# Optimization experiments

Measured on AMD Instinct MI355X. Metric: run time of the kernel, lower is better.

## Reference

```python
import jax, jax.numpy as jnp
import numpy as np
import math

FACTOR = 5


def setup_inputs() -> dict:
    key = jax.random.key(0)
    k1, k2, k3, k4 = jax.random.split(key, 4)
    B, L, H, D = 8, 1024, 8, 64
    S = FACTOR * math.ceil(math.log(L))  # U_part = 35
    return {
        "queries": jax.random.normal(k1, (B, L, H, D), jnp.float32),
        "keys": jax.random.normal(k2, (B, L, H, D), jnp.float32),
        "values": jax.random.normal(k3, (B, L, H, D), jnp.float32),
        "sample_idx": jax.random.randint(k4, (L, S), 0, L, dtype=jnp.int32),
        "attn_mask": 0,  # unused by the original forward
    }


def reference(queries, keys, values, sample_idx, attn_mask):
    B, L_Q, H, D = queries.shape
    L_K = keys.shape[1]
    # [B, L, H, D] -> [B, H, L, D]
    Q = jnp.transpose(queries, (0, 2, 1, 3))
    K = jnp.transpose(keys, (0, 2, 1, 3))
    V = jnpp_transpose(values) if False else jnp.transpose(values, (0, 2, 1, 3))

    u = min(FACTOR * math.ceil(math.log(L_Q)), L_Q)  # n_top

    # --- _prob_QK: sampled scores, sparsity measure, top-u query selection ---
    K_sample = K[:, :, sample_idx, :]  # [B, H, L_Q, S, D]
    QK_sample = jnp.einsum('bhqd,bhqsd->bhqs', Q, K_sample)  # [B, H, L_Q, S]
    M = QK_sample.max(axis=-1) - QK_sample.sum(axis=-1) / L_K  # [B, H, L_Q]
    _, M_top = jax.lax.top_k(M, u)  # [B, H, u]

    Q_reduce = jnp.take_along_axis(Q, M_top[..., None], axis=2)  # [B, H, u, D]
    scale = 1.0 / math.sqrt(D)
    scores_top = jnp.einsum('bhud,bhkd->bhuk', Q_reduce, K) * scale  # [B, H, u, L_K]

    # --- initial context (mask_flag=True): running causal mean of V ---
    denom = jnp.arange(1, L_K + 1, dtype=V.dtype)[:, None]  # [L_K, 1]
    context = jnp.cumsum(V, axis=2) / denom  # [B, H, L_K, D]

    # --- softmax over keys, sparse update of selected query rows ---
    attn = jax.nn.softmax(scores_top, axis=-1)  # [B, H, u, L_K]
    update = jnp.einsum('bhuk,bhkd->bhud', attn, V)  # [B, H, u, D]

    b_idx = jnp.arange(B)[:, None, None]
    h_idx = jnp.arange(H)[None, :, None]
    context = context.at[b_idx, h_idx, M_top].set(update)

    return jnp.transpose(context, (0, 2, 1, 3))  # [B, L_Q, H, D]
```

## Files before the change

### kernel.cpp

```cpp
#include <hip/hip_runtime.h>
#include <math.h>

#define BB 8
#define LL 1024
#define HH 8
#define DD 64
#define SS 35
#define UU 35
#define BH (BB*HH)
#define NCHK 4
#define CHK 256
#define RPAD 48

#define CSBLOCKS BH
#define MBLOCKS (BB*LL)

typedef __attribute__((ext_vector_type(8))) short short8;
typedef __attribute__((ext_vector_type(4))) float f32x4;

__device__ __forceinline__ size_t qkv_off(int b, int l, int h, int d) {
    return (((size_t)b*LL + l)*HH + h)*DD + d;
}

__device__ __forceinline__ unsigned short f2bf(float x) {
    unsigned int u = __float_as_uint(x);
    u = (u + 0x7fffu + ((u >> 16) & 1u)) >> 16;
    return (unsigned short)u;
}

__device__ __forceinline__ short8 ld_bf8_g(const float* __restrict__ p) {
    float4 x = *reinterpret_cast<const float4*>(p);
    float4 y = *reinterpret_cast<const float4*>(p + 4);
    short8 r;
    r[0] = (short)f2bf(x.x); r[1] = (short)f2bf(x.y);
    r[2] = (short)f2bf(x.z); r[3] = (short)f2bf(x.w);
    r[4] = (short)f2bf(y.x); r[5] = (short)f2bf(y.y);
    r[6] = (short)f2bf(y.z); r[7] = (short)f2bf(y.w);
    return r;
}

__device__ __forceinline__ float red8_shr(float p) {
    int t;
    t = __builtin_amdgcn_update_dpp(0, __float_as_int(p), 0x111, 0xF, 0xF, true);
    p += __int_as_float(t);
    t = __builtin_amdgcn_update_dpp(0, __float_as_int(p), 0x112, 0xF, 0xF, true);
    p += __int_as_float(t);
    t = __builtin_amdgcn_update_dpp(0, __float_as_int(p), 0x114, 0xF, 0xF, true);
    p += __int_as_float(t);
    return p;
}

__device__ __forceinline__ float wave_fmax64(float x) {
    int t;
    t = __builtin_amdgcn_update_dpp(0, __float_as_int(x), 0xB1, 0xF, 0xF, true);
    x = fmaxf(x, __int_as_float(t));
    t = __builtin_amdgcn_update_dpp(0, __float_as_int(x), 0x4E, 0xF, 0xF, true);
    x = fmaxf(x, __int_as_float(t));
    t = __builtin_amdgcn_update_dpp(0, __float_as_int(x), 0x141, 0xF, 0xF, true);
    x = fmaxf(x, __int_as_float(t));
    t = __builtin_amdgcn_update_dpp(0, __float_as_int(x), 0x140, 0xF, 0xF, true);
    x = fmaxf(x, __int_as_float(t));
    x = fmaxf(x, __shfl_xor(x, 16));
    x = fmaxf(x, __shfl_xor(x, 32));
    return x;
}

__device__ __forceinline__ int wave_imin64(int x) {
    int t;
    t = __builtin_amdgcn_update_dpp(0, x, 0xB1, 0xF, 0xF, true);  x = (t < x) ? t : x;
    t = __builtin_amdgcn_update_dpp(0, x, 0x4E, 0xF, 0xF, true);  x = (t < x) ? t : x;
    t = __builtin_amdgcn_update_dpp(0, x, 0x141, 0xF, 0xF, true); x = (t < x) ? t : x;
    t = __builtin_amdgcn_update_dpp(0, x, 0x140, 0xF, 0xF, true); x = (t < x) ? t : x;
    int y;
    y = __shfl_xor(x, 16); x = (y < x) ? y : x;
    y = __shfl_xor(x, 32); x = (y < x) ? y : x;
    return x;
}

__global__ __launch_bounds__(512, 2) void kernel_M_cumsum(const float* __restrict__ Q,
                                                          const float* __restrict__ K,
                                                          const float* __restrict__ V,
                                                          const int*   __restrict__ sidx,
                                                          float* __restrict__ M,
                                                          float* __restrict__ out) {
    int blk = blockIdx.x;
    if (blk < CSBLOCKS) {
        __shared__ float partial[8][64];
        int bh = blk;
        int b = bh >> 3, h = bh & 7;
        int d = threadIdx.x & 63, seg = threadIdx.x >> 6;
        int l0 = seg * 128;
        const float* vp = V + qkv_off(b, l0, h, d);

        float s = 0.f;
#pragma unroll 8
        for (int i = 0; i < 128; i++) s += vp[(size_t)i * (HH * DD)];
        partial[seg][d] = s;
        __syncthreads();
        float run = 0.f;
#pragma unroll
        for (int ss = 0; ss < 7; ss++) {
            float v = partial[ss][d];
            run += (ss < seg) ? v : 0.f;
        }
        float* op = out + qkv_off(b, l0, h, d);
#pragma unroll 8
        for (int i = 0; i < 128; i++) {
            run += vp[(size_t)i * (HH * DD)];
            op[(size_t)i * (HH * DD)] = run / (float)(l0 + i + 1);
        }
    } else {
        __shared__ float s_mx[8][8];
        __shared__ float s_sm[8][8];
        int mblk = blk - CSBLOCKS;
        int b = mblk & 7;
        int q = mblk >> 3;
        int tid = threadIdx.x;
        int w = tid >> 6, lane = tid & 63;
        int h = lane >> 3, j = lane & 7, dsub = j * 4;

        const float* qb = Q + ((size_t)(b * LL + q) * HH + h) * DD + dsub;
        f32x4 q0 = *reinterpret_cast<const f32x4*>(qb);
        f32x4 q1 = *reinterpret_cast<const f32x4*>(qb + 32);

        const int* sq = sidx + q * SS;
        int sl[5];
#pragma unroll
        for (int i = 0; i < 5; i++) {
            int s = w + 8 * i;
            sl[i] = sq[s < SS ? s : 0];
        }

        const float* kbase = K + (size_t)b * (LL * HH * DD) + h * DD + dsub;
        f32x4 ka[5], kc[5];
#pragma unroll
        for (int i = 0; i < 5; i++) {
            const float* kp = kbase + (size_t)sl[i] * (HH * DD);
            ka[i] = *reinterpret_cast<const f32x4*>(kp);
            kc[i] = *reinterpret_cast<const f32x4*>(kp + 32);
        }

        float mx = -INFINITY, sm = 0.f;
#pragma unroll
        for (int i = 0; i < 5; i++) {
            float d = q0.x * ka[i].x + q0.y * ka[i].y + q0.z * ka[i].z + q0.w * ka[i].w
                    + q1.x * kc[i].x + q1.y * kc[i].y + q1.z * kc[i].z + q1.w * kc[i].w;
            d = red8_shr(d);
            bool valid = (i < 4) || (w < 3);
            if (valid) { mx = fmaxf(mx, d); sm += d; }
        }
        if (j == 7) { s_mx[w][h] = mx; s_sm[w][h] = sm; }
        __syncthreads();
        if (tid < 8) {
            float m2 = -INFINITY, s2 = 0.f;
#pragma unroll
            for (int ww = 0; ww < 8; ww++) {
                m2 = fmaxf(m2, s_mx[ww][tid]);
                s2 += s_sm[ww][tid];
            }
            M[(b * HH + tid) * LL + q] = m2 - s2 * (1.0f / LL);
        }
    }
}

__global__ __launch_bounds__(256) void kernel_attn_part(const float* __restrict__ Q,
                                                        const float* __restrict__ K,
                                                        const float* __restrict__ V,
                                                        const float* __restrict__ M,
                                                        int*   __restrict__ top,
                                                        float* __restrict__ m_ws,
                                                        float* __restrict__ se_ws,
                                                        float* __restrict__ pv_ws) {
    __shared__ unsigned short vt[64 * CHK];
    __shared__ unsigned short p_lds[RPAD * CHK];
    __shared__ float red_m[4][RPAD];
    __shared__ float red_se[4][RPAD];
    __shared__ int   qpos_s[RPAD];

    const int blk = blockIdx.x;
    const int bh  = blk >> 2;
    const int ch  = blk & 3;
    const int b   = bh >> 3, h = bh & 7;
    const int l0  = ch * CHK;
    const int tid = threadIdx.x;
    const int w    = tid >> 6;
    const int lane = tid & 63;
    const int c    = lane & 15;
    const int g    = lane >> 4;
    const float scale = 0.125f;

    if (w == 0) {
        float v[16];
#pragma unroll
        for (int i = 0; i < 16; i++) v[i] = M[bh * LL + i * 64 + lane];
        int last = 0;
        for (int k = 0; k < UU; k++) {
            float bv = -INFINITY; int bslot = 0;
#pragma unroll
            for (int i = 0; i < 16; i++) {
                if (v[i] > bv) { bv = v[i]; bslot = i; }
            }
            float wm = wave_fmax64(bv);
            int gidx = (bv == wm) ? (bslot * 64 + lane) : 0x7fffffff;
            int widx = wave_imin64(gidx);
            if (lane == 0) qpos_s[k] = widx;
            if (k == UU - 1) last = widx;
            if ((widx & 63) == lane) {
                int slot = widx >> 6;
#pragma unroll
                for (int i = 0; i < 16; i++) if (i == slot) v[i] = -INFINITY;
            }
        }
        if (lane >= UU && lane < RPAD) qpos_s[lane] = last;
        if (ch == 0 && lane < UU) top[bh * UU + lane] = qpos_s[lane];
    } else {
        int t3 = tid - 64;
#pragma unroll
        for (int i = 0; i < 11; i++) {
            int task = i * 192 + t3;
            if (task < 2048) {
                int d   = task & 63;
                int lq8 = task >> 6;
                float vv[8];
#pragma unroll
                for (int jj = 0; jj < 8; jj++)
                    vv[jj] = V[qkv_off(b, l0 + lq8 * 8 + jj, h, d)];
                short8 pk;
#pragma unroll
                for (int jj = 0; jj < 8; jj++) pk[jj] = (short)f2bf(vv[jj]);
                *reinterpret_cast<short8*>(vt + d * CHK + (((lq8 ^ (d & 31)) << 3))) = pk;
            }
        }
    }
    __syncthreads();

    f32x4 acc[3][4];
#pragma unroll
    for (int mt = 0; mt < 3; mt++)
#pragma unroll
        for (int nt = 0; nt < 4; nt++) acc[mt][nt] = (f32x4){0.f, 0.f, 0.f, 0.f};

#pragma unroll
    for (int ks = 0; ks < 2; ks++) {
        int k0 = ks * 32 + g * 8;
        short8 af[3];
#pragma unroll
        for (int mt = 0; mt < 3; mt++) {
            int row = mt * 16 + c;
            af[mt] = ld_bf8_g(Q + qkv_off(b, qpos_s[row], h, k0));
        }
#pragma unroll
        for (int nt = 0; nt < 4; nt++) {
            int kl = l0 + w * 64 + nt * 16 + c;
            short8 bf = ld_bf8_g(K + qkv_off(b, kl, h, k0));
#pragma unroll
            for (int mt = 0; mt < 3; mt++)
                acc[mt][nt] = __builtin_amdgcn_mfma_f32_16x16x32_bf16(af[mt], bf, acc[mt][nt], 0, 0, 0);
        }
    }

    float tmax[3][4];
#pragma unroll
    for (int mt = 0; mt < 3; mt++)
#pragma unroll
        for (int r = 0; r < 4; r++) {
            float m = fmaxf(fmaxf(acc[mt][0][r], acc[mt][1][r]),
                            fmaxf(acc[mt][2][r], acc[mt][3][r]));
            m = fmaxf(m, __shfl_xor(m, 1));
            m = fmaxf(m, __shfl_xor(m, 2));
            m = fmaxf(m, __shfl_xor(m, 4));
            m = fmaxf(m, __shfl_xor(m, 8));
            tmax[mt][r] = m;
        }
    if (c == 0) {
#pragma unroll
        for (int mt = 0; mt < 3; mt++)
#pragma unroll
            for (int r = 0; r < 4; r++)
                red_m[w][mt * 16 + g * 4 + r] = tmax[mt][r];
    }
    __syncthreads();

    float tse[3][4];
#pragma unroll
    for (int mt = 0; mt < 3; mt++)
#pragma unroll
        for (int r = 0; r < 4; r++) {
            int row = mt * 16 + g * 4 + r;
            float m = fmaxf(fmaxf(red_m[0][row], red_m[1][row]),
                            fmaxf(red_m[2][row], red_m[3][row]));
            float s = 0.f;
#pragma unroll
            for (int nt = 0; nt < 4; nt++) {
                float p = __expf(scale * (acc[mt][nt][r] - m));
                acc[mt][nt][r] = p;
                s += p;
                p_lds[row * CHK + w * 64 + nt * 16 + c] = f2bf(p);
            }
            s += __shfl_xor(s, 1);
            s += __shfl_xor(s, 2);
            s += __shfl_xor(s, 4);
            s += __shfl_xor(s, 8);
            tse[mt][r] = s;
        }
    if (c == 0) {
#pragma unroll
        for (int mt = 0; mt < 3; mt++)
#pragma unroll
            for (int r = 0; r < 4; r++)
                red_se[w][mt * 16 + g * 4 + r] = tse[mt][r];
    }
    __syncthreads();

    if (tid < RPAD) {
        float mm = fmaxf(fmaxf(red_m[0][tid], red_m[1][tid]),
                         fmaxf(red_m[2][tid], red_m[3][tid]));
        float ss = red_se[0][tid] + red_se[1][tid] + red_se[2][tid] + red_se[3][tid];
        m_ws[blk * RPAD + tid]  = mm;
        se_ws[blk * RPAD + tid] = ss;
    }

    f32x4 acc2[3];
#pragma unroll
    for (int mt = 0; mt < 3; mt++) acc2[mt] = (f32x4){0.f, 0.f, 0.f, 0.f};

#pragma unroll
    for (int ks = 0; ks < 8; ks++) {
        int slot = ks * 4 + g;
        int d    = w * 16 + c;
        short8 bf = *reinterpret_cast<const short8*>(
            vt + d * CHK + ((slot ^ (d & 31)) << 3));
#pragma unroll
        for (int mt = 0; mt < 3; mt++) {
            short8 af = *reinterpret_cast<const short8*>(
                p_lds + (mt * 16 + c) * CHK + ks * 32 + g * 8);
            acc2[mt] = __builtin_amdgcn_mfma_f32_16x16x32_bf16(af, bf, acc2[mt], 0, 0, 0);
        }
    }

#pragma unroll
    for (int mt = 0; mt < 3; mt++)
#pragma unroll
        for (int r = 0; r < 4; r++) {
            int row = mt * 16 + g * 4 + r;
            pv_ws[((size_t)blk * RPAD + row) * 64 + w * 16 + c] = acc2[mt][r];
        }
}

__global__ __launch_bounds__(256) void kernel_attn_comb(const int* __restrict__ top,
                                                        const float* __restrict__ m_ws,
                                                        const float* __restrict__ se_ws,
                                                        const float* __restrict__ pv_ws,
                                                        float* __restrict__ out) {
    int bh = blockIdx.x;
    int b = bh >> 3, h = bh & 7;
    const float scale = 0.125f;
    for (int idx = threadIdx.x; idx < UU * 64; idx += 256) {
        int r = idx >> 6, d = idx & 63;
        float mc[NCHK];
        float mm = -INFINITY;
#pragma unroll
        for (int ch = 0; ch < NCHK; ch++) {
            mc[ch] = m_ws[(bh * NCHK + ch) * RPAD + r];
            mm = fmaxf(mm, mc[ch]);
        }
        float num = 0.f, den = 0.f;
#pragma unroll
        for (int ch = 0; ch < NCHK; ch++) {
            float f = __expf(scale * (mc[ch] - mm));
            num += f * pv_ws[((size_t)(bh * NCHK + ch) * RPAD + r) * 64 + d];
            den += f * se_ws[(bh * NCHK + ch) * RPAD + r];
        }
        out[qkv_off(b, top[bh * UU + r], h, d)] = num / den;
    }
}

extern "C" void kernel_launch(void* const* d_in, const int* in_sizes, int n_in,
                              void* d_out, int out_size, void* d_ws, size_t ws_size,
                              hipStream_t stream) {
    const float* Q    = (const float*)d_in[0];
    const float* K    = (const float*)d_in[1];
    const float* V    = (const float*)d_in[2];
    const int*   sidx = (const int*)d_in[3];
    float* out = (float*)d_out;

    char* ws = (char*)d_ws;
    float* M     = (float*)(ws);
    int*   top   = (int*)  (ws + 262144);
    float* m_ws  = (float*)(ws + 272384);
    float* se_ws = (float*)(ws + 321536);
    float* pv_ws = (float*)(ws + 370688);

    kernel_M_cumsum <<<CSBLOCKS + MBLOCKS, 512, 0, stream>>>(Q, K, V, sidx, M, out);
    kernel_attn_part<<<BH * NCHK, 256, 0, stream>>>(Q, K, V, M, top, m_ws, se_ws, pv_ws);
    kernel_attn_comb<<<BH, 256, 0, stream>>>(top, m_ws, se_ws, pv_ws, out);
}
```

Baseline: 68.22 us.

## Stage K chunks in LDS for sampled-score sparsity measure instead of global gathers

The sparsity-measure stage no longer launches one block per (batch, query) that gathers the 35 sampled K rows from global memory for every head. Each block now loads a 256-row K chunk for one (batch, head) into LDS. It then walks all 1024 queries, using a ballot to compact the sampled indices that fall inside its chunk, and writes a partial max and sum per chunk. The top-k stage merges the four partials per query into M. This removes a very large volume of random global/L2 traffic. The cost is a serial per-wave query loop, a large LDS footprint that may limit occupancy, and a larger workspace.

New measurement: 137.1 us. 101% more time.

```diff
diff --git a/kernel.cpp b/kernel.cpp
--- a/kernel.cpp
+++ b/kernel.cpp
@@ -11,9 +11,12 @@
 #define NCHK 4
 #define CHK 256
 #define RPAD 48
+#define NQU 4
+#define QROWS 256
+#define KSTR 68
 
 #define CSBLOCKS BH
-#define MBLOCKS (BB*LL)
+#define MBLOCKS (BH*NQU)
 
 typedef __attribute__((ext_vector_type(8))) short short8;
 typedef __attribute__((ext_vector_type(4))) float f32x4;
@@ -39,15 +42,13 @@
     return r;
 }
 
-__device__ __forceinline__ float red8_shr(float p) {
+__device__ __forceinline__ float red16_all(float d) {
     int t;
-    t = __builtin_amdgcn_update_dpp(0, __float_as_int(p), 0x111, 0xF, 0xF, true);
-    p += __int_as_float(t);
-    t = __builtin_amdgcn_update_dpp(0, __float_as_int(p), 0x112, 0xF, 0xF, true);
-    p += __int_as_float(t);
-    t = __builtin_amdgcn_update_dpp(0, __float_as_int(p), 0x114, 0xF, 0xF, true);
-    p += __int_as_float(t);
-    return p;
+    t = __builtin_amdgcn_update_dpp(0, __float_as_int(d), 0xB1, 0xF, 0xF, true);  d += __int_as_float(t);
+    t = __builtin_amdgcn_update_dpp(0, __float_as_int(d), 0x4E, 0xF, 0xF, true);  d += __int_as_float(t);
+    t = __builtin_amdgcn_update_dpp(0, __float_as_int(d), 0x141, 0xF, 0xF, true); d += __int_as_float(t);
+    t = __builtin_amdgcn_update_dpp(0, __float_as_int(d), 0x140, 0xF, 0xF, true); d += __int_as_float(t);
+    return d;
 }
 
 __device__ __forceinline__ float wave_fmax64(float x) {
@@ -81,7 +82,8 @@
                                                           const float* __restrict__ K,
                                                           const float* __restrict__ V,
                                                           const int*   __restrict__ sidx,
-                                                          float* __restrict__ M,
+                                                          float* __restrict__ m_mx,
+                                                          float* __restrict__ m_sm,
                                                           float* __restrict__ out) {
     int blk = blockIdx.x;
     if (blk < CSBLOCKS) {
@@ -110,55 +112,57 @@
             op[(size_t)i * (HH * DD)] = run / (float)(l0 + i + 1);
         }
     } else {
-        __shared__ float s_mx[8][8];
-        __shared__ float s_sm[8][8];
+        __shared__ float kq[QROWS * KSTR];
+        __shared__ int   crows[8][40];
         int mblk = blk - CSBLOCKS;
-        int b = mblk & 7;
-        int q = mblk >> 3;
+        int bh = mblk >> 2, qu = mblk & 3;
+        int b = bh >> 3, h = bh & 7;
+        int l0 = qu << 8;
         int tid = threadIdx.x;
         int w = tid >> 6, lane = tid & 63;
-        int h = lane >> 3, j = lane & 7, dsub = j * 4;
-
-        const float* qb = Q + ((size_t)(b * LL + q) * HH + h) * DD + dsub;
-        f32x4 q0 = *reinterpret_cast<const f32x4*>(qb);
-        f32x4 q1 = *reinterpret_cast<const f32x4*>(qb + 32);
-
-        const int* sq = sidx + q * SS;
-        int sl[5];
-#pragma unroll
-        for (int i = 0; i < 5; i++) {
-            int s = w + 8 * i;
-            sl[i] = sq[s < SS ? s : 0];
-        }
-
-        const float* kbase = K + (size_t)b * (LL * HH * DD) + h * DD + dsub;
-        f32x4 ka[5], kc[5];
-#pragma unroll
-        for (int i = 0; i < 5; i++) {
-            const float* kp = kbase + (size_t)sl[i] * (HH * DD);
-            ka[i] = *reinterpret_cast<const f32x4*>(kp);
-            kc[i] = *reinterpret_cast<const f32x4*>(kp + 32);
-        }
-
-        float mx = -INFINITY, sm = 0.f;
-#pragma unroll
-        for (int i = 0; i < 5; i++) {
-            float d = q0.x * ka[i].x + q0.y * ka[i].y + q0.z * ka[i].z + q0.w * ka[i].w
-                    + q1.x * kc[i].x + q1.y * kc[i].y + q1.z * kc[i].z + q1.w * kc[i].w;
-            d = red8_shr(d);
-            bool valid = (i < 4) || (w < 3);
-            if (valid) { mx = fmaxf(mx, d); sm += d; }
-        }
-        if (j == 7) { s_mx[w][h] = mx; s_sm[w][h] = sm; }
+        int jj = lane & 15, slot = lane >> 4;
+
+        const float* kbase = K + ((size_t)(b * LL + l0) * HH + h) * DD;
+#pragma unroll
+        for (int p = 0; p < 8; p++) {
+            int row = p * 32 + w * 4 + slot;
+            f32x4 kv = *reinterpret_cast<const f32x4*>(kbase + (size_t)row * (HH * DD) + jj * 4);
+            *reinterpret_cast<f32x4*>(kq + row * KSTR + jj * 4) = kv;
+        }
         __syncthreads();
-        if (tid < 8) {
-            float m2 = -INFINITY, s2 = 0.f;
-#pragma unroll
-            for (int ww = 0; ww < 8; ww++) {
-                m2 = fmaxf(m2, s_mx[ww][tid]);
-                s2 += s_sm[ww][tid];
-            }
-            M[(b * HH + tid) * LL + q] = m2 - s2 * (1.0f / LL);
+
+        for (int qi = 0; qi < 128; qi++) {
+            int q = (w << 7) + qi;
+            f32x4 q4 = *reinterpret_cast<const f32x4*>(
+                Q + ((size_t)(b * LL + q) * HH + h) * DD + jj * 4);
+
+            int s = lane < SS ? lane : SS - 1;
+            int idx = sidx[q * SS + s];
+            bool valid = (lane < SS) && (idx >= l0) && (idx < l0 + QROWS);
+            unsigned long long mask = __ballot(valid);
+            int cnt = __popcll(mask);
+            if (valid) {
+                int pos = __popcll(mask & ((1ull << lane) - 1ull));
+                crows[w][pos] = idx - l0;
+            }
+
+            float mx = -INFINITY, sm = 0.f;
+            int passes = (cnt + 3) >> 2;
+            for (int p = 0; p < passes; p++) {
+                int sp = p * 4 + slot;
+                bool sv = sp < cnt;
+                int r = crows[w][sv ? sp : 0];
+                f32x4 kv = *reinterpret_cast<const f32x4*>(kq + r * KSTR + jj * 4);
+                float d = q4.x * kv.x + q4.y * kv.y + q4.z * kv.z + q4.w * kv.w;
+                d = red16_all(d);
+                if (sv) { mx = fmaxf(mx, d); sm += d; }
+            }
+            mx = fmaxf(mx, __shfl_xor(mx, 16)); sm += __shfl_xor(sm, 16);
+            mx = fmaxf(mx, __shfl_xor(mx, 32)); sm += __shfl_xor(sm, 32);
+            if (lane == 0) {
+                m_mx[((size_t)mblk << 10) + q] = mx;
+                m_sm[((size_t)mblk << 10) + q] = sm;
+            }
         }
     }
 }
@@ -166,7 +170,8 @@
 __global__ __launch_bounds__(256) void kernel_attn_part(const float* __restrict__ Q,
                                                         const float* __restrict__ K,
                                                         const float* __restrict__ V,
-                                                        const float* __restrict__ M,
+                                                        const float* __restrict__ m_mx,
+                                                        const float* __restrict__ m_sm,
                                                         int*   __restrict__ top,
                                                         float* __restrict__ m_ws,
                                                         float* __restrict__ se_ws,
@@ -192,7 +197,15 @@
     if (w == 0) {
         float v[16];
 #pragma unroll
-        for (int i = 0; i < 16; i++) v[i] = M[bh * LL + i * 64 + lane];
+        for (int i = 0; i < 16; i++) {
+            int q = i * 64 + lane;
+            size_t base = ((size_t)bh << 12) + q;
+            float mx = fmaxf(fmaxf(m_mx[base], m_mx[base + 1024]),
+                             fmaxf(m_mx[base + 2048], m_mx[base + 3072]));
+            float sm = (m_sm[base] + m_sm[base + 1024])
+                     + (m_sm[base + 2048] + m_sm[base + 3072]);
+            v[i] = mx - sm * (1.0f / LL);
+        }
         int last = 0;
         for (int k = 0; k < UU; k++) {
             float bv = -INFINITY; int bslot = 0;
@@ -385,13 +398,14 @@
     float* out = (float*)d_out;
 
     char* ws = (char*)d_ws;
-    float* M     = (float*)(ws);
-    int*   top   = (int*)  (ws + 262144);
-    float* m_ws  = (float*)(ws + 272384);
-    float* se_ws = (float*)(ws + 321536);
-    float* pv_ws = (float*)(ws + 370688);
-
-    kernel_M_cumsum <<<CSBLOCKS + MBLOCKS, 512, 0, stream>>>(Q, K, V, sidx, M, out);
-    kernel_attn_part<<<BH * NCHK, 256, 0, stream>>>(Q, K, V, M, top, m_ws, se_ws, pv_ws);
+    float* m_mx  = (float*)(ws);
+    float* m_sm  = (float*)(ws + 1048576);
+    int*   top   = (int*)  (ws + 2097152);
+    float* m_ws  = (float*)(ws + 2107392);
+    float* se_ws = (float*)(ws + 2156544);
+    float* pv_ws = (float*)(ws + 2205696);
+
+    kernel_M_cumsum <<<CSBLOCKS + MBLOCKS, 512, 0, stream>>>(Q, K, V, sidx, m_mx, m_sm, out);
+    kernel_attn_part<<<BH * NCHK, 256, 0, stream>>>(Q, K, V, m_mx, m_sm, top, m_ws, se_ws, pv_ws);
     kernel_attn_comb<<<BH, 256, 0, stream>>>(top, m_ws, se_ws, pv_ws, out);
 }
```
